# Kernel optimization log

Measured on AMD Instinct MI355X. Metric: run time of the kernel, lower is better.

The kernel has to match this reference:

```python
import jax, jax.numpy as jnp
import numpy as np

H, K, D, HID, B = 8, 2048, 64, 1024, 8192
TEMP = 1.0
LN_EPS = 1e-5


def setup_inputs() -> dict:
    key = jax.random.key(0)
    ks = jax.random.split(key, 6)
    s = lambda k, shape, scale=0.02: jax.random.normal(k, shape, jnp.float32) * scale
    return dict(
        z=jax.random.normal(ks[0], (B, HID), jnp.float32),
        w1=s(ks[1], (H, HID, 2 * D)),
        b1=jnp.zeros((H, 2 * D), jnp.float32),
        w2=s(ks[2], (H, 2 * D, D)),
        b2=jnp.zeros((H, D), jnp.float32),
        ln_g=jnp.ones((H, D), jnp.float32),
        ln_b=jnp.zeros((H, D), jnp.float32),
        codebooks=jax.random.normal(ks[3], (H, K, D), jnp.float32) * 0.1,
        dec_w=s(ks[4], (H, D, HID // H)),
        dec_b=jnp.zeros((H, HID // H), jnp.float32),
    )


def reference(z, w1, b1, w2, b2, ln_g, ln_b, codebooks, dec_w, dec_b):
    sg = jax.lax.stop_gradient
    Bf = z.shape[0]
    # per-head projection MLP (all heads fused via einsum): [B,HID] -> [B,H,2D] -> [B,H,D]
    h1 = jax.nn.gelu(jnp.einsum('bi,hio->bho', z, w1) + b1, approximate=False)
    zh = jnp.einsum('bho,hod->bhd', h1, w2) + b2
    mu = zh.mean(-1, keepdims=True)
    var = zh.var(-1, keepdims=True)  # biased, as torch LayerNorm
    z_heads = (zh - mu) / jnp.sqrt(var + LN_EPS) * ln_g + ln_b  # [B,H,D]
    # squared-distance to codebooks: ||z||^2 + ||c||^2 - 2 z.c  -> [B,H,K]
    z_sq = (z_heads ** 2).sum(-1)[..., None]          # [B,H,1]
    c_sq = (codebooks ** 2).sum(-1)[None]             # [1,H,K]
    zc = jnp.einsum('bhd,hkd->bhk', z_heads, codebooks)
    dists = z_sq + c_sq - 2.0 * zc
    idx = jnp.argmin(dists, axis=-1)                  # [B,H] int
    z_q = codebooks[jnp.arange(H)[None, :], idx]      # gather -> [B,H,D]
    # per-head decoders then concat -> [B,HID]
    dec = lambda x: (jnp.einsum('bhd,hdo->bho', x, dec_w) + dec_b).reshape(Bf, -1)
    z_q_dec = dec(z_q)
    z_proj = dec(z_heads)
    z_q_st = z_proj + sg(z_q_dec - z_proj)
    commit = jnp.mean((z_proj - sg(z_q_dec)) ** 2)
    codebook_loss = jnp.mean((sg(z_proj) - z_q_dec) ** 2)
    # entropy regularizer over soft assignment probs
    probs = jax.nn.softmax(-dists * TEMP, axis=-1)    # [B,H,K]
    avg_probs = probs.mean(0)                         # [H,K]
    entropy = -(avg_probs * jnp.log(avg_probs + 1e-8)).sum(-1).mean()
    entropy_loss = 1.0 - entropy / np.float32(np.log(K))
    # orthogonality: pairwise co-occurrence deviation from independence
    p = jnp.zeros((H, K), jnp.float32).at[jnp.arange(H)[None, :], idx].add(1.0) / Bf  # [H,K]
    ortho = jnp.float32(0.0)
    cnt = 0
    for i in range(H):
        for j in range(i + 1, H):
            co = jnp.zeros((K, K), jnp.float32).at[idx[:, i], idx[:, j]].add(1.0) / (Bf + 1e-8)
            expected = p[i][:, None] * p[j][None, :]
            ortho = ortho + jnp.mean(jnp.abs(co - expected))
            cnt += 1
    ortho = ortho / cnt
    return z_q_st, idx, commit, codebook_loss, entropy_loss, ortho, sg(z_heads)
```

## Files before the change

kernel.cpp:

```cpp
#include <hip/hip_runtime.h>
#include <math.h>

#define H 8
#define KK 2048
#define DD 64
#define HIDN 1024
#define BB 8192
#define TWO_D 128
#define OO 128

#define WS_CSQ   1048576
#define WS_ZSQ   1064960
#define WS_IDX   1130496
#define WS_AVGP  1196032
#define WS_HIST  1212416
#define WS_ACC   1228800
#define WS_ZERO_BYTES ((16384 + 16384 + 4) * 4)

#define OUT_ZQ 0
#define OUT_IDX 8388608
#define OUT_COMMIT 8454144
#define OUT_CBL 8454145
#define OUT_ENT 8454146
#define OUT_ORTHO 8454147
#define OUT_ZH 8454148
#define W2P_OFF 3145728

typedef __attribute__((ext_vector_type(8))) short bf16x8;
typedef __attribute__((ext_vector_type(4))) float f32x4;

__device__ inline unsigned short bf16_rne(float x) {
    union { float f; unsigned u; } c; c.f = x;
    unsigned r = c.u + 0x7FFFu + ((c.u >> 16) & 1u);
    return (unsigned short)(r >> 16);
}
__device__ inline float bf16_f32(unsigned short h) {
    union { unsigned u; float f; } c; c.u = ((unsigned)h) << 16;
    return c.f;
}
__device__ inline void split3(float x, short* hh, short* mm, short* ll) {
    unsigned short h_ = bf16_rne(x);
    float r1 = x - bf16_f32(h_);
    unsigned short m_ = bf16_rne(r1);
    float r2 = r1 - bf16_f32(m_);
    unsigned short l_ = bf16_rne(r2);
    *hh = (short)h_; *mm = (short)m_; *ll = (short)l_;
}

__device__ inline void gload_lds16(const void* g, void* l) {
    __builtin_amdgcn_global_load_lds(
        (const __attribute__((address_space(1))) unsigned int*)g,
        (__attribute__((address_space(3))) unsigned int*)l, 16, 0, 0);
}

__global__ __launch_bounds__(256) void k_pre_w1(const float* __restrict__ w1, float* outp) {
    short* w1p = (short*)outp;
    int h = blockIdx.x >> 5, kc = blockIdx.x & 31;
    int t = threadIdx.x;
    int l = t & 63, w = t >> 6;
    int lb = l & 15, lg = l >> 4;
#pragma unroll
    for (int oi = 0; oi < 2; ++oi) {
        int ot = w + oi * 4;
        union { short e[8]; bf16x8 v; } uh, um, ul;
#pragma unroll
        for (int j = 0; j < 8; ++j) {
            float x = w1[(size_t)(h * HIDN + kc * 32 + lg * 8 + j) * TWO_D + ot * 16 + lb];
            split3(x, &uh.e[j], &um.e[j], &ul.e[j]);
        }
        size_t base = (((size_t)(h * 32 + kc) * 8 + ot) * 3) * 512 + l * 8;
        *(bf16x8*)(w1p + base) = uh.v;
        *(bf16x8*)(w1p + base + 512) = um.v;
        *(bf16x8*)(w1p + base + 1024) = ul.v;
    }
}

__global__ __launch_bounds__(256) void k_pre_w2(const float* __restrict__ w2, float* outp) {
    short* w2p = (short*)outp + W2P_OFF;
    int h = blockIdx.x;
    int t = threadIdx.x;
    int l = t & 63, w = t >> 6;
    int lb = l & 15, lg = l >> 4;
#pragma unroll
    for (int i = 0; i < 4; ++i) {
        int fr = w * 4 + i;
        int dt = fr >> 2, oc = fr & 3;
        union { short e[8]; bf16x8 v; } uh, um, ul;
#pragma unroll
        for (int j = 0; j < 8; ++j) {
            float x = w2[(size_t)(h * TWO_D + oc * 32 + lg * 8 + j) * DD + dt * 16 + lb];
            split3(x, &uh.e[j], &um.e[j], &ul.e[j]);
        }
        size_t base = (((size_t)(h * 4 + dt) * 4 + oc) * 3) * 512 + l * 8;
        *(bf16x8*)(w2p + base) = uh.v;
        *(bf16x8*)(w2p + base + 512) = um.v;
        *(bf16x8*)(w2p + base + 1024) = ul.v;
    }
}

__global__ __launch_bounds__(256) void k_pre(const float* __restrict__ cb, float* __restrict__ ws) {
    int h = blockIdx.x >> 3, kb = blockIdx.x & 7;
    int t = threadIdx.x;
    int l = t & 63;
    int lb = l & 15, lg = l >> 4;
    short* stg = (short*)ws;
#pragma unroll
    for (int p = 0; p < 4; ++p) {
        int T = kb * 16 + p * 4 + (t >> 6);
        int k = T * 16 + lb;
        const float* row = cb + (size_t)(h * KK + k) * DD;
        float4 a0 = *(const float4*)(row + lg * 8);
        float4 a1 = *(const float4*)(row + lg * 8 + 4);
        float4 c0 = *(const float4*)(row + 32 + lg * 8);
        float4 c1 = *(const float4*)(row + 32 + lg * 8 + 4);
        float v0[8] = {a0.x, a0.y, a0.z, a0.w, a1.x, a1.y, a1.z, a1.w};
        float v1[8] = {c0.x, c0.y, c0.z, c0.w, c1.x, c1.y, c1.z, c1.w};
        union { short e[8]; bf16x8 v; } h0, h1;
        float s = 0.f;
#pragma unroll
        for (int j = 0; j < 8; ++j) {
            float x = v0[j];
            s = fmaf(x, x, s);
            h0.e[j] = (short)bf16_rne(x);
            float y = v1[j];
            s = fmaf(y, y, s);
            h1.e[j] = (short)bf16_rne(y);
        }
        size_t base = ((size_t)(h * 128 + T)) * 1024 + l * 8;
        *(bf16x8*)(stg + base) = h0.v;
        *(bf16x8*)(stg + base + 512) = h1.v;
        s += __shfl_xor(s, 16);
        s += __shfl_xor(s, 32);
        if (lg == 0) ws[WS_CSQ + h * KK + k] = s;
    }
}

__global__ __launch_bounds__(512, 4) void k1(const float* __restrict__ z, const float* __restrict__ b1,
                                             const float* __restrict__ b2, const float* __restrict__ lng,
                                             const float* __restrict__ lnb, float* out,
                                             float* __restrict__ ws) {
    __shared__ char SM[51200];
    int t = threadIdx.x;
    int h = blockIdx.y;
    int b0 = blockIdx.x * 64;
    int w = t >> 6, l = t & 63;
    int rg = w >> 1, wc = w & 1;
    int lb = l & 15, lg = l >> 4;

    const short* w2p = (const short*)out + W2P_OFF;
    const char* w1h = (const char*)out + (size_t)h * (32 * 24576);
    const float* zrow = z + (size_t)(b0 + rg * 16 + lb) * HIDN + lg * 8;

    {
        char* lb0 = SM + (t >> 6) * 1024;
        const char* gb = w1h + t * 16;
#pragma unroll
        for (int r = 0; r < 3; ++r) gload_lds16(gb + r * 8192, lb0 + r * 8192);
#pragma unroll
        for (int r = 0; r < 3; ++r) gload_lds16(gb + 24576 + r * 8192, lb0 + 24576 + r * 8192);
    }
    float4 zA = *(const float4*)(zrow);
    float4 zB = *(const float4*)(zrow + 4);
    __syncthreads();

    f32x4 acc[4];
#pragma unroll
    for (int i = 0; i < 4; ++i) acc[i] = (f32x4){0.f, 0.f, 0.f, 0.f};

#pragma unroll
    for (int c = 0; c < 32; ++c) {
        if (c > 0) {
            if (c < 31) asm volatile("s_waitcnt vmcnt(3)" ::: "memory");
            else        asm volatile("s_waitcnt vmcnt(0)" ::: "memory");
            __builtin_amdgcn_sched_barrier(0);
            __builtin_amdgcn_s_barrier();
            __builtin_amdgcn_sched_barrier(0);
        }
        {
            float zc[8] = {zA.x, zA.y, zA.z, zA.w, zB.x, zB.y, zB.z, zB.w};
            union { short e[8]; bf16x8 v; } uh, um, ul;
#pragma unroll
            for (int j = 0; j < 8; ++j) split3(zc[j], &uh.e[j], &um.e[j], &ul.e[j]);
            bf16x8 bh = uh.v, bm = um.v, blo = ul.v;
            const char* bp = SM + (c & 1) * 24576;
#pragma unroll
            for (int ot = 0; ot < 4; ++ot) {
                const char* fb = bp + (wc * 4 + ot) * 3072 + l * 16;
                bf16x8 ah = *(const bf16x8*)(fb);
                bf16x8 am = *(const bf16x8*)(fb + 1024);
                bf16x8 al = *(const bf16x8*)(fb + 2048);
                f32x4 cc = acc[ot];
                cc = __builtin_amdgcn_mfma_f32_16x16x32_bf16(ah, bh, cc, 0, 0, 0);
                cc = __builtin_amdgcn_mfma_f32_16x16x32_bf16(ah, bm, cc, 0, 0, 0);
                cc = __builtin_amdgcn_mfma_f32_16x16x32_bf16(am, bh, cc, 0, 0, 0);
                cc = __builtin_amdgcn_mfma_f32_16x16x32_bf16(ah, blo, cc, 0, 0, 0);
                cc = __builtin_amdgcn_mfma_f32_16x16x32_bf16(al, bh, cc, 0, 0, 0);
                cc = __builtin_amdgcn_mfma_f32_16x16x32_bf16(am, bm, cc, 0, 0, 0);
                acc[ot] = cc;
            }
        }
        __builtin_amdgcn_sched_barrier(0);
        __builtin_amdgcn_s_barrier();
        __builtin_amdgcn_sched_barrier(0);
        if (c < 31) {
            zA = *(const float4*)(zrow + (c + 1) * 32);
            zB = *(const float4*)(zrow + (c + 1) * 32 + 4);
        }
        if (c + 2 < 32) {
            char* lb0 = SM + (c & 1) * 24576 + (t >> 6) * 1024;
            const char* gb = w1h + (size_t)(c + 2) * 24576 + t * 16;
#pragma unroll
            for (int r = 0; r < 3; ++r) gload_lds16(gb + r * 8192, lb0 + r * 8192);
        }
    }
    __syncthreads();

    float* h1L = (float*)SM;
    float* zhL = (float*)(SM + 33792);

#pragma unroll
    for (int ot = 0; ot < 4; ++ot)
#pragma unroll
        for (int r = 0; r < 4; ++r) {
            int o = (wc * 4 + ot) * 16 + lg * 4 + r;
            float x = acc[ot][r] + b1[h * TWO_D + o];
            float gl = 0.5f * x * (1.0f + erff(x * 0.70710678118654752f));
            h1L[(rg * 16 + lb) * 132 + o] = gl;
        }
    __syncthreads();

    f32x4 a2[2];
    a2[0] = (f32x4){0.f, 0.f, 0.f, 0.f};
    a2[1] = (f32x4){0.f, 0.f, 0.f, 0.f};
#pragma unroll
    for (int oc = 0; oc < 4; ++oc) {
        const float* hr = h1L + (rg * 16 + lb) * 132 + oc * 32 + lg * 8;
        union { short e[8]; bf16x8 v; } uh, um, ul;
#pragma unroll
        for (int j = 0; j < 8; ++j) split3(hr[j], &uh.e[j], &um.e[j], &ul.e[j]);
        bf16x8 bh = uh.v, bm = um.v, blo = ul.v;
#pragma unroll
        for (int dti = 0; dti < 2; ++dti) {
            int dt = wc * 2 + dti;
            const short* fb = w2p + (((size_t)(h * 4 + dt) * 4 + oc) * 3) * 512 + l * 8;
            bf16x8 ah = *(const bf16x8*)(fb);
            bf16x8 am = *(const bf16x8*)(fb + 512);
            bf16x8 al = *(const bf16x8*)(fb + 1024);
            f32x4 cc = a2[dti];
            cc = __builtin_amdgcn_mfma_f32_16x16x32_bf16(ah, bh, cc, 0, 0, 0);
            cc = __builtin_amdgcn_mfma_f32_16x16x32_bf16(ah, bm, cc, 0, 0, 0);
            cc = __builtin_amdgcn_mfma_f32_16x16x32_bf16(am, bh, cc, 0, 0, 0);
            cc = __builtin_amdgcn_mfma_f32_16x16x32_bf16(ah, blo, cc, 0, 0, 0);
            cc = __builtin_amdgcn_mfma_f32_16x16x32_bf16(al, bh, cc, 0, 0, 0);
            cc = __builtin_amdgcn_mfma_f32_16x16x32_bf16(am, bm, cc, 0, 0, 0);
            a2[dti] = cc;
        }
    }
#pragma unroll
    for (int dti = 0; dti < 2; ++dti)
#pragma unroll
        for (int r = 0; r < 4; ++r) {
            int d = (wc * 2 + dti) * 16 + lg * 4 + r;
            zhL[(rg * 16 + lb) * 68 + d] = a2[dti][r] + b2[h * DD + d];
        }
    __syncthreads();

    {
        int row = t >> 3, c0 = (t & 7) * 8;
        const float* zr = zhL + row * 68 + c0;
        float v[8];
#pragma unroll
        for (int j = 0; j < 8; ++j) v[j] = zr[j];
        float s = 0.f;
#pragma unroll
        for (int j = 0; j < 8; ++j) s += v[j];
        s += __shfl_xor(s, 1); s += __shfl_xor(s, 2); s += __shfl_xor(s, 4);
        float mu = s * (1.0f / 64.0f);
        float vv = 0.f;
#pragma unroll
        for (int j = 0; j < 8; ++j) { float d = v[j] - mu; vv = fmaf(d, d, vv); }
        vv += __shfl_xor(vv, 1); vv += __shfl_xor(vv, 2); vv += __shfl_xor(vv, 4);
        float rstd = 1.0f / sqrtf(vv * (1.0f / 64.0f) + 1e-5f);
        float zn[8]; float ss = 0.f;
#pragma unroll
        for (int j = 0; j < 8; ++j) {
            float x = (v[j] - mu) * rstd * lng[h * DD + c0 + j] + lnb[h * DD + c0 + j];
            zn[j] = x; ss = fmaf(x, x, ss);
        }
        ss += __shfl_xor(ss, 1); ss += __shfl_xor(ss, 2); ss += __shfl_xor(ss, 4);
        int brow = b0 + row;
        if ((t & 7) == 0) ws[WS_ZSQ + brow * H + h] = ss;
        float4 s0 = {zn[0], zn[1], zn[2], zn[3]};
        float4 s1 = {zn[4], zn[5], zn[6], zn[7]};
        *(float4*)(out + OUT_ZH + (size_t)(brow * H + h) * DD + c0) = s0;
        *(float4*)(out + OUT_ZH + (size_t)(brow * H + h) * DD + c0 + 4) = s1;
    }
}

#define MARGIN 0.10f
__device__ inline void stage16(const char* gsrc, short* lbuf, int t) {
    char* lb_ = (char*)lbuf + (t >> 6) * 1024;
    gload_lds16(gsrc + t * 16, lb_);
}
__global__ __launch_bounds__(1024, 4) void k2(const float* __restrict__ cb,
                                              float* __restrict__ out, float* __restrict__ ws) {
    __shared__ short bufs[3][8192];
    __shared__ float zt[32][68];
    __shared__ float csqL[2048];
    __shared__ float zsqL[32];
    __shared__ float redM[8][32], redS[8][32], redE[8][32];
    __shared__ int   redK[8][32];
    __shared__ float MbL[32], SbL[32];
    __shared__ float paccL[2048];

    int t = threadIdx.x;
    int h = blockIdx.y;
    int b0 = blockIdx.x * 32;
    int w = t >> 6, l = t & 63;
    int rg = w >> 3, kg = w & 7;
    int lb = l & 15, lg = l >> 4;
    int rmy = rg * 16 + lb;

    const char* stgbase = (const char*)ws + (size_t)h * 262144;

    stage16(stgbase, bufs[0], t);
    stage16(stgbase + 16384, bufs[1], t);
    stage16(stgbase + 32768, bufs[2], t);
    for (int i = t; i < 2048; i += 1024) {
        paccL[i] = 0.f;
        csqL[i] = ws[WS_CSQ + h * KK + i];
    }
#pragma unroll
    for (int i = 0; i < 2; ++i) {
        int q = t + i * 1024;
        int r = q >> 6, d = q & 63;
        zt[r][d] = out[OUT_ZH + (size_t)((b0 + r) * H + h) * DD + d];
    }
    if (t < 32) zsqL[t] = ws[WS_ZSQ + (b0 + t) * H + h];
    __syncthreads();

    bf16x8 bh[2], bl[2];
#pragma unroll
    for (int s = 0; s < 2; ++s) {
        const float* zr = &zt[rmy][s * 32 + lg * 8];
        union { short e[8]; bf16x8 v; } uh, ul;
#pragma unroll
        for (int j = 0; j < 8; ++j) {
            float x = zr[j];
            unsigned short hb = bf16_rne(x);
            uh.e[j] = (short)hb;
            ul.e[j] = (short)bf16_rne(x - bf16_f32(hb));
        }
        bh[s] = uh.v; bl[s] = ul.v;
    }

    f32x4 acc[16];
#pragma unroll
    for (int a = 0; a < 16; ++a) acc[a] = (f32x4){0.f, 0.f, 0.f, 0.f};

#pragma unroll
    for (int c = 0; c < 16; ++c) {
        if (c > 0) {
            if (c <= 13)      asm volatile("s_waitcnt vmcnt(2)" ::: "memory");
            else if (c == 14) asm volatile("s_waitcnt vmcnt(1)" ::: "memory");
            else              asm volatile("s_waitcnt vmcnt(0)" ::: "memory");
            __builtin_amdgcn_sched_barrier(0);
            __builtin_amdgcn_s_barrier();
            __builtin_amdgcn_sched_barrier(0);
        }
        {
            const short* fb = bufs[c % 3] + kg * 1024 + l * 8;
            bf16x8 C0 = *(const bf16x8*)(fb);
            bf16x8 C1 = *(const bf16x8*)(fb + 512);
            f32x4 cc = acc[c];
            cc = __builtin_amdgcn_mfma_f32_16x16x32_bf16(bh[0], C0, cc, 0, 0, 0);
            cc = __builtin_amdgcn_mfma_f32_16x16x32_bf16(bl[0], C0, cc, 0, 0, 0);
            cc = __builtin_amdgcn_mfma_f32_16x16x32_bf16(bh[1], C1, cc, 0, 0, 0);
            cc = __builtin_amdgcn_mfma_f32_16x16x32_bf16(bl[1], C1, cc, 0, 0, 0);
            acc[c] = cc;
        }
        if (c < 15) {
            __builtin_amdgcn_sched_barrier(0);
            __builtin_amdgcn_s_barrier();
            __builtin_amdgcn_sched_barrier(0);
            if (c + 3 < 16)
                stage16(stgbase + (size_t)(c + 3) * 16384, bufs[c % 3], t);
        }
    }

    float zsqv[4];
#pragma unroll
    for (int r = 0; r < 4; ++r) zsqv[r] = zsqL[rg * 16 + lg * 4 + r];
    float mn[4] = {3.4e38f, 3.4e38f, 3.4e38f, 3.4e38f};
#pragma unroll
    for (int ai = 0; ai < 16; ++ai) {
        float cs = csqL[(8 * ai + kg) * 16 + lb];
        f32x4 a = acc[ai];
        f32x4 d;
#pragma unroll
        for (int r = 0; r < 4; ++r) {
            float dv = (zsqv[r] + cs) - 2.f * a[r];
            d[r] = dv;
            mn[r] = fminf(mn[r], dv);
        }
        acc[ai] = d;
    }
#pragma unroll
    for (int off = 1; off < 16; off <<= 1)
#pragma unroll
        for (int r = 0; r < 4; ++r) mn[r] = fminf(mn[r], __shfl_xor(mn[r], off));
    if (lb == 0)
#pragma unroll
        for (int r = 0; r < 4; ++r) redM[kg][rg * 16 + lg * 4 + r] = mn[r];
    __syncthreads();
    if (t < 32) {
        float m = redM[0][t];
#pragma unroll
        for (int g = 1; g < 8; ++g) m = fminf(m, redM[g][t]);
        MbL[t] = m;
    }
    __syncthreads();
    float Mb[4];
#pragma unroll
    for (int r = 0; r < 4; ++r) Mb[r] = MbL[rg * 16 + lg * 4 + r];

    float S[4] = {0.f, 0.f, 0.f, 0.f};
    unsigned mk0 = 0, mk1 = 0, mk2 = 0, mk3 = 0;
#pragma unroll
    for (int ai = 0; ai < 16; ++ai) {
        f32x4 d = acc[ai];
        f32x4 e;
#pragma unroll
        for (int r = 0; r < 4; ++r) {
            float dv = d[r];
            float ev = __expf(Mb[r] - dv);
            S[r] += ev;
            e[r] = ev;
            bool cand = dv <= Mb[r] + MARGIN;
            if (r == 0) mk0 |= cand ? (1u << ai) : 0u;
            if (r == 1) mk1 |= cand ? (1u << ai) : 0u;
            if (r == 2) mk2 |= cand ? (1u << ai) : 0u;
            if (r == 3) mk3 |= cand ? (1u << ai) : 0u;
        }
        acc[ai] = e;
    }
#pragma unroll
    for (int off = 1; off < 16; off <<= 1)
#pragma unroll
        for (int r = 0; r < 4; ++r) S[r] += __shfl_xor(S[r], off);
    if (lb == 0)
#pragma unroll
        for (int r = 0; r < 4; ++r) redS[kg][rg * 16 + lg * 4 + r] = S[r];

    float eB[4] = {3.4e38f, 3.4e38f, 3.4e38f, 3.4e38f};
    int kB[4] = {0x7FFFFFFF, 0x7FFFFFFF, 0x7FFFFFFF, 0x7FFFFFFF};
#pragma unroll
    for (int r = 0; r < 4; ++r) {
        unsigned m = (r == 0) ? mk0 : (r == 1) ? mk1 : (r == 2) ? mk2 : mk3;
        const float* zr0 = &zt[rg * 16 + lg * 4 + r][0];
        float eBest = 3.4e38f; int kBest = 0x7FFFFFFF;
        while (m) {
            int ai = (int)__ffs(m) - 1;
            m &= m - 1;
            int k = (8 * ai + kg) * 16 + lb;
            const float4* crow = (const float4*)(cb + (size_t)(h * KK + k) * DD);
            float s = 0.f;
#pragma unroll 1
            for (int q = 0; q < 16; ++q) {
                float4 cv = crow[q];
                s = fmaf(zr0[q * 4 + 0], cv.x, s);
                s = fmaf(zr0[q * 4 + 1], cv.y, s);
                s = fmaf(zr0[q * 4 + 2], cv.z, s);
                s = fmaf(zr0[q * 4 + 3], cv.w, s);
            }
            float ex = (zsqv[r] + csqL[k]) - 2.f * s;
            if (ex < eBest || (ex == eBest && k < kBest)) { eBest = ex; kBest = k; }
        }
        eB[r] = eBest; kB[r] = kBest;
    }
#pragma unroll
    for (int off = 1; off < 16; off <<= 1)
#pragma unroll
        for (int r = 0; r < 4; ++r) {
            float oe = __shfl_xor(eB[r], off);
            int ok = __shfl_xor(kB[r], off);
            if (oe < eB[r] || (oe == eB[r] && ok < kB[r])) { eB[r] = oe; kB[r] = ok; }
        }
    if (lb == 0)
#pragma unroll
        for (int r = 0; r < 4; ++r) {
            redE[kg][rg * 16 + lg * 4 + r] = eB[r];
            redK[kg][rg * 16 + lg * 4 + r] = kB[r];
        }
    __syncthreads();
    if (t < 32) {
        float Sv = redS[0][t];
#pragma unroll
        for (int g = 1; g < 8; ++g) Sv += redS[g][t];
        SbL[t] = Sv;
        float e0 = redE[0][t]; int k0_ = redK[0][t];
#pragma unroll
        for (int g = 1; g < 8; ++g) {
            float oe = redE[g][t]; int ok = redK[g][t];
            if (oe < e0 || (oe == e0 && ok < k0_)) { e0 = oe; k0_ = ok; }
        }
        out[OUT_IDX + (b0 + t) * H + h] = (float)k0_;
        ((int*)ws)[WS_IDX + (b0 + t) * H + h] = k0_;
        atomicAdd(((unsigned*)ws) + WS_HIST + h * KK + k0_, 1u);
    }
    __syncthreads();
    float invS[4];
#pragma unroll
    for (int r = 0; r < 4; ++r) invS[r] = 1.0f / SbL[rg * 16 + lg * 4 + r];

#pragma unroll
    for (int ai = 0; ai < 16; ++ai) {
        f32x4 e = acc[ai];
        float v = e[0] * invS[0];
        v = fmaf(e[1], invS[1], v);
        v = fmaf(e[2], invS[2], v);
        v = fmaf(e[3], invS[3], v);
        v += __shfl_xor(v, 16);
        v += __shfl_xor(v, 32);
        if (lg == 0) atomicAdd(&paccL[(8 * ai + kg) * 16 + lb], v);
    }
    __syncthreads();
    for (int i = t; i < 2048; i += 1024)
        atomicAdd(ws + WS_AVGP + h * KK + i, paccL[i]);
}

__global__ __launch_bounds__(256, 2) void k3(const float* __restrict__ cb, const float* __restrict__ dw,
                                             const float* __restrict__ db, float* __restrict__ out,
                                             float* __restrict__ ws) {
    __shared__ float zqt[32][65];
    __shared__ float zht[32][65];
    __shared__ float dwt[64][128];
    __shared__ int idxs[32];
    __shared__ double redc[4];
    int t = threadIdx.x;
    int h = blockIdx.y;
    int b0 = blockIdx.x * 32;
    if (t < 32) idxs[t] = ((const int*)ws)[WS_IDX + (b0 + t) * H + h];
    __syncthreads();
#pragma unroll
    for (int p = 0; p < 8; ++p) {
        int q = t + 256 * p;
        int r = q >> 6, d = q & 63;
        zqt[r][d] = cb[(size_t)(h * KK + idxs[r]) * DD + d];
        zht[r][d] = out[OUT_ZH + (size_t)((b0 + r) * H + h) * DD + d];
    }
#pragma unroll
    for (int p = 0; p < 8; ++p) {
        int q = t + 256 * p;
        int r = q >> 5, c4 = q & 31;
        *(float4*)(&dwt[r][c4 * 4]) = *(const float4*)(dw + (size_t)(h * DD + r) * OO + c4 * 4);
    }
    __syncthreads();
    int rg = t >> 4, cg = t & 15;
    float aq[2][8], ap[2][8];
#pragma unroll
    for (int i = 0; i < 2; ++i)
#pragma unroll
        for (int j = 0; j < 8; ++j) { aq[i][j] = 0.f; ap[i][j] = 0.f; }
#pragma unroll 4
    for (int d = 0; d < 64; ++d) {
        float q0 = zqt[rg * 2][d], q1 = zqt[rg * 2 + 1][d];
        float p0 = zht[rg * 2][d], p1 = zht[rg * 2 + 1][d];
        float4 wa = *(const float4*)(&dwt[d][cg * 8]);
        float4 wb = *(const float4*)(&dwt[d][cg * 8 + 4]);
        float ww[8] = {wa.x, wa.y, wa.z, wa.w, wb.x, wb.y, wb.z, wb.w};
#pragma unroll
        for (int j = 0; j < 8; ++j) {
            aq[0][j] = fmaf(q0, ww[j], aq[0][j]);
            aq[1][j] = fmaf(q1, ww[j], aq[1][j]);
            ap[0][j] = fmaf(p0, ww[j], ap[0][j]);
            ap[1][j] = fmaf(p1, ww[j], ap[1][j]);
        }
    }
    float lsum = 0.f;
#pragma unroll
    for (int i = 0; i < 2; ++i) {
        float vq4[8];
#pragma unroll
        for (int j = 0; j < 8; ++j) {
            float bb = db[h * OO + cg * 8 + j];
            float vq = aq[i][j] + bb;
            float vp = ap[i][j] + bb;
            vq4[j] = vp + (vq - vp);
            float e = vp - vq;
            lsum = fmaf(e, e, lsum);
        }
        float4 s0 = {vq4[0], vq4[1], vq4[2], vq4[3]};
        float4 s1 = {vq4[4], vq4[5], vq4[6], vq4[7]};
        size_t o = (size_t)(b0 + rg * 2 + i) * HIDN + h * OO + cg * 8;
        *(float4*)(out + OUT_ZQ + o) = s0;
        *(float4*)(out + OUT_ZQ + o + 4) = s1;
    }
#pragma unroll
    for (int off = 1; off < 64; off <<= 1) lsum += __shfl_xor(lsum, off);
    if ((t & 63) == 0) redc[t >> 6] = (double)lsum;
    __syncthreads();
    if (t == 0) atomicAdd((double*)(ws + WS_ACC), redc[0] + redc[1] + redc[2] + redc[3]);
}

__global__ __launch_bounds__(256) void k6(float* __restrict__ ws) {
    __shared__ unsigned slots[16384];
    __shared__ unsigned cnts[16384];
    int t = threadIdx.x;
    int bid = blockIdx.x;
    int pi = 0, pj = 1;
    {
        int c = 0;
        for (int a = 0; a < H; ++a)
            for (int b = a + 1; b < H; ++b) { if (c == bid) { pi = a; pj = b; } ++c; }
    }
    for (int s = t; s < 16384; s += 256) { slots[s] = 0xFFFFFFFFu; cnts[s] = 0u; }
    __syncthreads();
    const int* idxi = ((const int*)ws) + WS_IDX;
    for (int b = t; b < BB; b += 256) {
        unsigned key = ((unsigned)idxi[b * H + pi] << 11) | (unsigned)idxi[b * H + pj];
        unsigned p = (key * 2654435761u) >> 18;
        while (true) {
            unsigned old = atomicCAS(&slots[p], 0xFFFFFFFFu, key);
            if (old == 0xFFFFFFFFu || old == key) { atomicAdd(&cnts[p], 1u); break; }
            p = (p + 1) & 16383u;
        }
    }
    __syncthreads();
    const unsigned* hist = ((const unsigned*)ws) + WS_HIST;
    double loc = 0.0;
    for (int s = t; s < 16384; s += 256) {
        unsigned key = slots[s];
        if (key != 0xFFFFFFFFu) {
            int ki = (int)(key >> 11), kj = (int)(key & 2047u);
            float c = (float)cnts[s] * (1.0f / 8192.0f);
            float piv = (float)hist[pi * KK + ki] * (1.0f / 8192.0f);
            float pjv = (float)hist[pj * KK + kj] * (1.0f / 8192.0f);
            float e = piv * pjv;
            loc += (double)fabsf(c - e) - (double)e;
        }
    }
    double spi = 0.0, spj = 0.0;
    for (int k = t; k < KK; k += 256) {
        spi += (double)hist[pi * KK + k];
        spj += (double)hist[pj * KK + k];
    }
#pragma unroll
    for (int off = 1; off < 64; off <<= 1) {
        loc += __shfl_xor(loc, off);
        spi += __shfl_xor(spi, off);
        spj += __shfl_xor(spj, off);
    }
    __syncthreads();
    double* sc = (double*)cnts;
    if ((t & 63) == 0) { int w = t >> 6; sc[w] = loc; sc[4 + w] = spi; sc[8 + w] = spj; }
    __syncthreads();
    if (t == 0) {
        double L = sc[0] + sc[1] + sc[2] + sc[3];
        double SPI = (sc[4] + sc[5] + sc[6] + sc[7]) / 8192.0;
        double SPJ = (sc[8] + sc[9] + sc[10] + sc[11]) / 8192.0;
        atomicAdd(((double*)(ws + WS_ACC)) + 1, L + SPI * SPJ);
    }
}

__global__ __launch_bounds__(256) void k4(float* __restrict__ out, float* __restrict__ ws) {
    __shared__ double red[256];
    int t = threadIdx.x;
    double tot = 0.0;
    for (int h = 0; h < H; ++h) {
        double s = 0.0;
        for (int k = t; k < KK; k += 256) {
            double a = (double)ws[WS_AVGP + h * KK + k] / 8192.0;
            s += a * log(a + 1e-8);
        }
        tot += s;
    }
    red[t] = tot;
    __syncthreads();
    for (int off = 128; off; off >>= 1) {
        if (t < off) red[t] += red[t + off];
        __syncthreads();
    }
    if (t == 0) {
        double entropy = -red[0] / 8.0;
        out[OUT_ENT] = (float)(1.0 - entropy / log(2048.0));
        double ca = *(const double*)(ws + WS_ACC);
        float cm = (float)(ca / (8192.0 * 1024.0));
        out[OUT_COMMIT] = cm;
        out[OUT_CBL] = cm;
        double oa = *(((const double*)(ws + WS_ACC)) + 1);
        out[OUT_ORTHO] = (float)(oa / (28.0 * 4194304.0));
    }
}

extern "C" void kernel_launch(void* const* d_in, const int* in_sizes, int n_in,
                              void* d_out, int out_size, void* d_ws, size_t ws_size,
                              hipStream_t stream) {
    (void)in_sizes; (void)n_in; (void)out_size; (void)ws_size;
    const float* z   = (const float*)d_in[0];
    const float* w1  = (const float*)d_in[1];
    const float* b1  = (const float*)d_in[2];
    const float* w2  = (const float*)d_in[3];
    const float* b2  = (const float*)d_in[4];
    const float* lng = (const float*)d_in[5];
    const float* lnb = (const float*)d_in[6];
    const float* cb  = (const float*)d_in[7];
    const float* dw  = (const float*)d_in[8];
    const float* db  = (const float*)d_in[9];
    float* out = (float*)d_out;
    float* ws = (float*)d_ws;

    hipMemsetAsync(ws + WS_AVGP, 0, WS_ZERO_BYTES, stream);
    k_pre_w1<<<256, 256, 0, stream>>>(w1, out);
    k_pre_w2<<<8, 256, 0, stream>>>(w2, out);
    k_pre<<<64, 256, 0, stream>>>(cb, ws);
    k1<<<dim3(128, 8), 512, 0, stream>>>(z, b1, b2, lng, lnb, out, ws);
    k2<<<dim3(256, 8), 1024, 0, stream>>>(cb, out, ws);
    k3<<<dim3(256, 8), 256, 0, stream>>>(cb, dw, db, out, ws);
    k6<<<28, 256, 0, stream>>>(ws);
    k4<<<1, 256, 0, stream>>>(out, ws);
}
```

Before: 537.4 us.

## Shrink k2 blocks to 16 rows, drop LDS staging, move histogram to separate kernel

The distance/argmin kernel now uses 512-thread blocks covering 16 batch rows, with twice as many blocks. Each thread issues two async loads per stage, and the staged codebook layout is permuted so each wave owns a contiguous 256-code range. Codebook norms are read from global memory instead of an LDS copy, the LDS soft-probability accumulator is replaced by direct global atomics, and the MFMA block runs at raised priority. The per-row global histogram atomics move into a new per-head kernel with an LDS histogram. This lowers LDS use and raises occupancy, but the codebook is re-streamed once per block for half as many rows, so staged codebook traffic doubles, global atomics increase, and one more launch is added.

```diff
diff --git a/kernel.cpp b/kernel.cpp
--- a/kernel.cpp
+++ b/kernel.cpp
@@ -126,7 +126,8 @@
             s = fmaf(y, y, s);
             h1.e[j] = (short)bf16_rne(y);
         }
-        size_t base = ((size_t)(h * 128 + T)) * 1024 + l * 8;
+        int off = (T & 15) * 8 + (T >> 4);
+        size_t base = ((size_t)(h * 128 + off)) * 1024 + l * 8;
         *(bf16x8*)(stg + base) = h0.v;
         *(bf16x8*)(stg + base + 512) = h1.v;
         s += __shfl_xor(s, 16);
@@ -298,51 +299,45 @@
 }
 
 #define MARGIN 0.10f
-__device__ inline void stage16(const char* gsrc, short* lbuf, int t) {
+__device__ inline void stage16k(const char* gsrc, short* lbuf, int t) {
     char* lb_ = (char*)lbuf + (t >> 6) * 1024;
-    gload_lds16(gsrc + t * 16, lb_);
-}
-__global__ __launch_bounds__(1024, 4) void k2(const float* __restrict__ cb,
-                                              float* __restrict__ out, float* __restrict__ ws) {
+    const char* gb = gsrc + t * 16;
+    gload_lds16(gb, lb_);
+    gload_lds16(gb + 8192, lb_ + 8192);
+}
+__global__ __launch_bounds__(512, 4) void k2(const float* __restrict__ cb,
+                                             float* __restrict__ out, float* __restrict__ ws) {
     __shared__ short bufs[3][8192];
-    __shared__ float zt[32][68];
-    __shared__ float csqL[2048];
-    __shared__ float zsqL[32];
-    __shared__ float redM[8][32], redS[8][32], redE[8][32];
-    __shared__ int   redK[8][32];
-    __shared__ float MbL[32], SbL[32];
-    __shared__ float paccL[2048];
+    __shared__ float zt[16][68];
+    __shared__ float redM[8][16], redS[8][16], redE[8][16];
+    __shared__ int   redK[8][16];
+    __shared__ float MbL[16], SbL[16];
+    __shared__ float zsqL[16];
 
     int t = threadIdx.x;
     int h = blockIdx.y;
-    int b0 = blockIdx.x * 32;
-    int w = t >> 6, l = t & 63;
-    int rg = w >> 3, kg = w & 7;
+    int b0 = blockIdx.x * 16;
+    int kg = t >> 6, l = t & 63;
     int lb = l & 15, lg = l >> 4;
-    int rmy = rg * 16 + lb;
 
     const char* stgbase = (const char*)ws + (size_t)h * 262144;
 
-    stage16(stgbase, bufs[0], t);
-    stage16(stgbase + 16384, bufs[1], t);
-    stage16(stgbase + 32768, bufs[2], t);
-    for (int i = t; i < 2048; i += 1024) {
-        paccL[i] = 0.f;
-        csqL[i] = ws[WS_CSQ + h * KK + i];
-    }
+    stage16k(stgbase, bufs[0], t);
+    stage16k(stgbase + 16384, bufs[1], t);
+    stage16k(stgbase + 32768, bufs[2], t);
 #pragma unroll
     for (int i = 0; i < 2; ++i) {
-        int q = t + i * 1024;
+        int q = t + i * 512;
         int r = q >> 6, d = q & 63;
         zt[r][d] = out[OUT_ZH + (size_t)((b0 + r) * H + h) * DD + d];
     }
-    if (t < 32) zsqL[t] = ws[WS_ZSQ + (b0 + t) * H + h];
-    __syncthreads();
-
-    bf16x8 bh[2], bl[2];
+    if (t < 16) zsqL[t] = ws[WS_ZSQ + (b0 + t) * H + h];
+    __syncthreads();
+
+    bf16x8 bh[2], blo[2];
 #pragma unroll
     for (int s = 0; s < 2; ++s) {
-        const float* zr = &zt[rmy][s * 32 + lg * 8];
+        const float* zr = &zt[lb][s * 32 + lg * 8];
         union { short e[8]; bf16x8 v; } uh, ul;
 #pragma unroll
         for (int j = 0; j < 8; ++j) {
@@ -351,7 +346,7 @@
             uh.e[j] = (short)hb;
             ul.e[j] = (short)bf16_rne(x - bf16_f32(hb));
         }
-        bh[s] = uh.v; bl[s] = ul.v;
+        bh[s] = uh.v; blo[s] = ul.v;
     }
 
     f32x4 acc[16];
@@ -361,8 +356,8 @@
 #pragma unroll
     for (int c = 0; c < 16; ++c) {
         if (c > 0) {
-            if (c <= 13)      asm volatile("s_waitcnt vmcnt(2)" ::: "memory");
-            else if (c == 14) asm volatile("s_waitcnt vmcnt(1)" ::: "memory");
+            if (c <= 13)      asm volatile("s_waitcnt vmcnt(4)" ::: "memory");
+            else if (c == 14) asm volatile("s_waitcnt vmcnt(2)" ::: "memory");
             else              asm volatile("s_waitcnt vmcnt(0)" ::: "memory");
             __builtin_amdgcn_sched_barrier(0);
             __builtin_amdgcn_s_barrier();
@@ -373,10 +368,12 @@
             bf16x8 C0 = *(const bf16x8*)(fb);
             bf16x8 C1 = *(const bf16x8*)(fb + 512);
             f32x4 cc = acc[c];
+            __builtin_amdgcn_s_setprio(1);
             cc = __builtin_amdgcn_mfma_f32_16x16x32_bf16(bh[0], C0, cc, 0, 0, 0);
-            cc = __builtin_amdgcn_mfma_f32_16x16x32_bf16(bl[0], C0, cc, 0, 0, 0);
+            cc = __builtin_amdgcn_mfma_f32_16x16x32_bf16(blo[0], C0, cc, 0, 0, 0);
             cc = __builtin_amdgcn_mfma_f32_16x16x32_bf16(bh[1], C1, cc, 0, 0, 0);
-            cc = __builtin_amdgcn_mfma_f32_16x16x32_bf16(bl[1], C1, cc, 0, 0, 0);
+            cc = __builtin_amdgcn_mfma_f32_16x16x32_bf16(blo[1], C1, cc, 0, 0, 0);
+            __builtin_amdgcn_s_setprio(0);
             acc[c] = cc;
         }
         if (c < 15) {
@@ -384,17 +381,17 @@
             __builtin_amdgcn_s_barrier();
             __builtin_amdgcn_sched_barrier(0);
             if (c + 3 < 16)
-                stage16(stgbase + (size_t)(c + 3) * 16384, bufs[c % 3], t);
+                stage16k(stgbase + (size_t)(c + 3) * 16384, bufs[c % 3], t);
         }
     }
 
     float zsqv[4];
 #pragma unroll
-    for (int r = 0; r < 4; ++r) zsqv[r] = zsqL[rg * 16 + lg * 4 + r];
+    for (int r = 0; r < 4; ++r) zsqv[r] = zsqL[lg * 4 + r];
     float mn[4] = {3.4e38f, 3.4e38f, 3.4e38f, 3.4e38f};
 #pragma unroll
     for (int ai = 0; ai < 16; ++ai) {
-        float cs = csqL[(8 * ai + kg) * 16 + lb];
+        float cs = ws[WS_CSQ + h * KK + kg * 256 + ai * 16 + lb];
         f32x4 a = acc[ai];
         f32x4 d;
 #pragma unroll
@@ -411,9 +408,9 @@
         for (int r = 0; r < 4; ++r) mn[r] = fminf(mn[r], __shfl_xor(mn[r], off));
     if (lb == 0)
 #pragma unroll
-        for (int r = 0; r < 4; ++r) redM[kg][rg * 16 + lg * 4 + r] = mn[r];
-    __syncthreads();
-    if (t < 32) {
+        for (int r = 0; r < 4; ++r) redM[kg][lg * 4 + r] = mn[r];
+    __syncthreads();
+    if (t < 16) {
         float m = redM[0][t];
 #pragma unroll
         for (int g = 1; g < 8; ++g) m = fminf(m, redM[g][t]);
@@ -422,7 +419,7 @@
     __syncthreads();
     float Mb[4];
 #pragma unroll
-    for (int r = 0; r < 4; ++r) Mb[r] = MbL[rg * 16 + lg * 4 + r];
+    for (int r = 0; r < 4; ++r) Mb[r] = MbL[lg * 4 + r];
 
     float S[4] = {0.f, 0.f, 0.f, 0.f};
     unsigned mk0 = 0, mk1 = 0, mk2 = 0, mk3 = 0;
@@ -450,19 +447,19 @@
         for (int r = 0; r < 4; ++r) S[r] += __shfl_xor(S[r], off);
     if (lb == 0)
 #pragma unroll
-        for (int r = 0; r < 4; ++r) redS[kg][rg * 16 + lg * 4 + r] = S[r];
+        for (int r = 0; r < 4; ++r) redS[kg][lg * 4 + r] = S[r];
 
     float eB[4] = {3.4e38f, 3.4e38f, 3.4e38f, 3.4e38f};
     int kB[4] = {0x7FFFFFFF, 0x7FFFFFFF, 0x7FFFFFFF, 0x7FFFFFFF};
 #pragma unroll
     for (int r = 0; r < 4; ++r) {
         unsigned m = (r == 0) ? mk0 : (r == 1) ? mk1 : (r == 2) ? mk2 : mk3;
-        const float* zr0 = &zt[rg * 16 + lg * 4 + r][0];
+        const float* zr0 = &zt[lg * 4 + r][0];
         float eBest = 3.4e38f; int kBest = 0x7FFFFFFF;
         while (m) {
             int ai = (int)__ffs(m) - 1;
             m &= m - 1;
-            int k = (8 * ai + kg) * 16 + lb;
+            int k = kg * 256 + ai * 16 + lb;
             const float4* crow = (const float4*)(cb + (size_t)(h * KK + k) * DD);
             float s = 0.f;
 #pragma unroll 1
@@ -473,7 +470,7 @@
                 s = fmaf(zr0[q * 4 + 2], cv.z, s);
                 s = fmaf(zr0[q * 4 + 3], cv.w, s);
             }
-            float ex = (zsqv[r] + csqL[k]) - 2.f * s;
+            float ex = (zsqv[r] + ws[WS_CSQ + h * KK + k]) - 2.f * s;
             if (ex < eBest || (ex == eBest && k < kBest)) { eBest = ex; kBest = k; }
         }
         eB[r] = eBest; kB[r] = kBest;
@@ -489,11 +486,11 @@
     if (lb == 0)
 #pragma unroll
         for (int r = 0; r < 4; ++r) {
-            redE[kg][rg * 16 + lg * 4 + r] = eB[r];
-            redK[kg][rg * 16 + lg * 4 + r] = kB[r];
-        }
-    __syncthreads();
-    if (t < 32) {
+            redE[kg][lg * 4 + r] = eB[r];
+            redK[kg][lg * 4 + r] = kB[r];
+        }
+    __syncthreads();
+    if (t < 16) {
         float Sv = redS[0][t];
 #pragma unroll
         for (int g = 1; g < 8; ++g) Sv += redS[g][t];
@@ -506,12 +503,11 @@
         }
         out[OUT_IDX + (b0 + t) * H + h] = (float)k0_;
         ((int*)ws)[WS_IDX + (b0 + t) * H + h] = k0_;
-        atomicAdd(((unsigned*)ws) + WS_HIST + h * KK + k0_, 1u);
     }
     __syncthreads();
     float invS[4];
 #pragma unroll
-    for (int r = 0; r < 4; ++r) invS[r] = 1.0f / SbL[rg * 16 + lg * 4 + r];
+    for (int r = 0; r < 4; ++r) invS[r] = 1.0f / SbL[lg * 4 + r];
 
 #pragma unroll
     for (int ai = 0; ai < 16; ++ai) {
@@ -522,11 +518,22 @@
         v = fmaf(e[3], invS[3], v);
         v += __shfl_xor(v, 16);
         v += __shfl_xor(v, 32);
-        if (lg == 0) atomicAdd(&paccL[(8 * ai + kg) * 16 + lb], v);
-    }
-    __syncthreads();
-    for (int i = t; i < 2048; i += 1024)
-        atomicAdd(ws + WS_AVGP + h * KK + i, paccL[i]);
+        if (lg == 0)
+            atomicAdd(ws + WS_AVGP + h * KK + kg * 256 + ai * 16 + lb, v);
+    }
+}
+
+__global__ __launch_bounds__(256) void k_hist(float* __restrict__ ws) {
+    __shared__ unsigned hl[2048];
+    int h = blockIdx.x, t = threadIdx.x;
+    for (int i = t; i < 2048; i += 256) hl[i] = 0u;
+    __syncthreads();
+    const int* idxi = ((const int*)ws) + WS_IDX;
+    for (int b = t; b < BB; b += 256)
+        atomicAdd(&hl[idxi[b * H + h]], 1u);
+    __syncthreads();
+    for (int i = t; i < 2048; i += 256)
+        ((unsigned*)ws)[WS_HIST + h * KK + i] = hl[i];
 }
 
 __global__ __launch_bounds__(256, 2) void k3(const float* __restrict__ cb, const float* __restrict__ dw,
@@ -715,7 +722,8 @@
     k_pre_w2<<<8, 256, 0, stream>>>(w2, out);
     k_pre<<<64, 256, 0, stream>>>(cb, ws);
     k1<<<dim3(128, 8), 512, 0, stream>>>(z, b1, b2, lng, lnb, out, ws);
-    k2<<<dim3(256, 8), 1024, 0, stream>>>(cb, out, ws);
+    k2<<<dim3(512, 8), 512, 0, stream>>>(cb, out, ws);
+    k_hist<<<8, 256, 0, stream>>>(ws);
     k3<<<dim3(256, 8), 256, 0, stream>>>(cb, dw, db, out, ws);
     k6<<<28, 256, 0, stream>>>(ws);
     k4<<<1, 256, 0, stream>>>(out, ws);
```

After: 568.3 us. 5.7% more time.

## Load split-bf16 codebook fragments directly to registers and move histogram to separate kernel

Applied to the files above, without the earlier changes.

The codebook distance kernel stops staging codebook tiles through LDS with barriers. Each wave now reads pre-split hi/lo bf16 fragments straight from global memory into registers with a two-deep prefetch, and adds a third MFMA term (z_hi·c_lo) to raise precision, which allows a tighter refinement margin. The soft-probability accumulation moves ahead of the exact argmin refinement, and the global histogram atomics are replaced by a small per-head shared-memory histogram kernel. In exchange the staging buffer doubles, MFMA work per tile grows by half, and csq is read from global memory instead of LDS.

```diff
diff --git a/kernel.cpp b/kernel.cpp
--- a/kernel.cpp
+++ b/kernel.cpp
@@ -115,20 +115,26 @@
         float4 c1 = *(const float4*)(row + 32 + lg * 8 + 4);
         float v0[8] = {a0.x, a0.y, a0.z, a0.w, a1.x, a1.y, a1.z, a1.w};
         float v1[8] = {c0.x, c0.y, c0.z, c0.w, c1.x, c1.y, c1.z, c1.w};
-        union { short e[8]; bf16x8 v; } h0, h1;
+        union { short e[8]; bf16x8 v; } h0, h1, l0, l1;
         float s = 0.f;
 #pragma unroll
         for (int j = 0; j < 8; ++j) {
             float x = v0[j];
             s = fmaf(x, x, s);
-            h0.e[j] = (short)bf16_rne(x);
+            unsigned short hb = bf16_rne(x);
+            h0.e[j] = (short)hb;
+            l0.e[j] = (short)bf16_rne(x - bf16_f32(hb));
             float y = v1[j];
             s = fmaf(y, y, s);
-            h1.e[j] = (short)bf16_rne(y);
-        }
-        size_t base = ((size_t)(h * 128 + T)) * 1024 + l * 8;
+            unsigned short hb2 = bf16_rne(y);
+            h1.e[j] = (short)hb2;
+            l1.e[j] = (short)bf16_rne(y - bf16_f32(hb2));
+        }
+        size_t base = ((size_t)(h * 128 + T)) * 2048 + l * 8;
         *(bf16x8*)(stg + base) = h0.v;
         *(bf16x8*)(stg + base + 512) = h1.v;
+        *(bf16x8*)(stg + base + 1024) = l0.v;
+        *(bf16x8*)(stg + base + 1536) = l1.v;
         s += __shfl_xor(s, 16);
         s += __shfl_xor(s, 32);
         if (lg == 0) ws[WS_CSQ + h * KK + k] = s;
@@ -297,21 +303,15 @@
     }
 }
 
-#define MARGIN 0.10f
-__device__ inline void stage16(const char* gsrc, short* lbuf, int t) {
-    char* lb_ = (char*)lbuf + (t >> 6) * 1024;
-    gload_lds16(gsrc + t * 16, lb_);
-}
+#define MARGIN 0.05f
 __global__ __launch_bounds__(1024, 4) void k2(const float* __restrict__ cb,
                                               float* __restrict__ out, float* __restrict__ ws) {
-    __shared__ short bufs[3][8192];
     __shared__ float zt[32][68];
-    __shared__ float csqL[2048];
-    __shared__ float zsqL[32];
+    __shared__ float paccL[2048];
     __shared__ float redM[8][32], redS[8][32], redE[8][32];
     __shared__ int   redK[8][32];
     __shared__ float MbL[32], SbL[32];
-    __shared__ float paccL[2048];
+    __shared__ float zsqL[32];
 
     int t = threadIdx.x;
     int h = blockIdx.y;
@@ -321,15 +321,7 @@
     int lb = l & 15, lg = l >> 4;
     int rmy = rg * 16 + lb;
 
-    const char* stgbase = (const char*)ws + (size_t)h * 262144;
-
-    stage16(stgbase, bufs[0], t);
-    stage16(stgbase + 16384, bufs[1], t);
-    stage16(stgbase + 32768, bufs[2], t);
-    for (int i = t; i < 2048; i += 1024) {
-        paccL[i] = 0.f;
-        csqL[i] = ws[WS_CSQ + h * KK + i];
-    }
+    for (int i = t; i < 2048; i += 1024) paccL[i] = 0.f;
 #pragma unroll
     for (int i = 0; i < 2; ++i) {
         int q = t + i * 1024;
@@ -339,7 +331,7 @@
     if (t < 32) zsqL[t] = ws[WS_ZSQ + (b0 + t) * H + h];
     __syncthreads();
 
-    bf16x8 bh[2], bl[2];
+    bf16x8 bh[2], blo[2];
 #pragma unroll
     for (int s = 0; s < 2; ++s) {
         const float* zr = &zt[rmy][s * 32 + lg * 8];
@@ -351,40 +343,41 @@
             uh.e[j] = (short)hb;
             ul.e[j] = (short)bf16_rne(x - bf16_f32(hb));
         }
-        bh[s] = uh.v; bl[s] = ul.v;
-    }
+        bh[s] = uh.v; blo[s] = ul.v;
+    }
+
+    const short* tbase = (const short*)ws + ((size_t)(h * 128 + kg * 16)) * 2048 + l * 8;
 
     f32x4 acc[16];
 #pragma unroll
     for (int a = 0; a < 16; ++a) acc[a] = (f32x4){0.f, 0.f, 0.f, 0.f};
 
-#pragma unroll
-    for (int c = 0; c < 16; ++c) {
-        if (c > 0) {
-            if (c <= 13)      asm volatile("s_waitcnt vmcnt(2)" ::: "memory");
-            else if (c == 14) asm volatile("s_waitcnt vmcnt(1)" ::: "memory");
-            else              asm volatile("s_waitcnt vmcnt(0)" ::: "memory");
-            __builtin_amdgcn_sched_barrier(0);
-            __builtin_amdgcn_s_barrier();
-            __builtin_amdgcn_sched_barrier(0);
-        }
-        {
-            const short* fb = bufs[c % 3] + kg * 1024 + l * 8;
-            bf16x8 C0 = *(const bf16x8*)(fb);
-            bf16x8 C1 = *(const bf16x8*)(fb + 512);
-            f32x4 cc = acc[c];
-            cc = __builtin_amdgcn_mfma_f32_16x16x32_bf16(bh[0], C0, cc, 0, 0, 0);
-            cc = __builtin_amdgcn_mfma_f32_16x16x32_bf16(bl[0], C0, cc, 0, 0, 0);
-            cc = __builtin_amdgcn_mfma_f32_16x16x32_bf16(bh[1], C1, cc, 0, 0, 0);
-            cc = __builtin_amdgcn_mfma_f32_16x16x32_bf16(bl[1], C1, cc, 0, 0, 0);
-            acc[c] = cc;
-        }
-        if (c < 15) {
-            __builtin_amdgcn_sched_barrier(0);
-            __builtin_amdgcn_s_barrier();
-            __builtin_amdgcn_sched_barrier(0);
-            if (c + 3 < 16)
-                stage16(stgbase + (size_t)(c + 3) * 16384, bufs[c % 3], t);
+    bf16x8 c0h, c1h, c0l, c1l, p0h, p1h, p0l, p1l;
+    c0h = *(const bf16x8*)(tbase);
+    c1h = *(const bf16x8*)(tbase + 512);
+    c0l = *(const bf16x8*)(tbase + 1024);
+    c1l = *(const bf16x8*)(tbase + 1536);
+    p0h = *(const bf16x8*)(tbase + 2048);
+    p1h = *(const bf16x8*)(tbase + 2048 + 512);
+    p0l = *(const bf16x8*)(tbase + 2048 + 1024);
+    p1l = *(const bf16x8*)(tbase + 2048 + 1536);
+#pragma unroll
+    for (int ai = 0; ai < 16; ++ai) {
+        f32x4 cc = acc[ai];
+        cc = __builtin_amdgcn_mfma_f32_16x16x32_bf16(bh[0], c0h, cc, 0, 0, 0);
+        cc = __builtin_amdgcn_mfma_f32_16x16x32_bf16(blo[0], c0h, cc, 0, 0, 0);
+        cc = __builtin_amdgcn_mfma_f32_16x16x32_bf16(bh[0], c0l, cc, 0, 0, 0);
+        cc = __builtin_amdgcn_mfma_f32_16x16x32_bf16(bh[1], c1h, cc, 0, 0, 0);
+        cc = __builtin_amdgcn_mfma_f32_16x16x32_bf16(blo[1], c1h, cc, 0, 0, 0);
+        cc = __builtin_amdgcn_mfma_f32_16x16x32_bf16(bh[1], c1l, cc, 0, 0, 0);
+        acc[ai] = cc;
+        c0h = p0h; c1h = p1h; c0l = p0l; c1l = p1l;
+        if (ai + 2 < 16) {
+            const short* np = tbase + (size_t)(ai + 2) * 2048;
+            p0h = *(const bf16x8*)(np);
+            p1h = *(const bf16x8*)(np + 512);
+            p0l = *(const bf16x8*)(np + 1024);
+            p1l = *(const bf16x8*)(np + 1536);
         }
     }
 
@@ -394,7 +387,7 @@
     float mn[4] = {3.4e38f, 3.4e38f, 3.4e38f, 3.4e38f};
 #pragma unroll
     for (int ai = 0; ai < 16; ++ai) {
-        float cs = csqL[(8 * ai + kg) * 16 + lb];
+        float cs = ws[WS_CSQ + h * KK + (kg * 16 + ai) * 16 + lb];
         f32x4 a = acc[ai];
         f32x4 d;
 #pragma unroll
@@ -451,6 +444,30 @@
     if (lb == 0)
 #pragma unroll
         for (int r = 0; r < 4; ++r) redS[kg][rg * 16 + lg * 4 + r] = S[r];
+    __syncthreads();
+    if (t < 32) {
+        float Sv = redS[0][t];
+#pragma unroll
+        for (int g = 1; g < 8; ++g) Sv += redS[g][t];
+        SbL[t] = Sv;
+    }
+    __syncthreads();
+    float invS[4];
+#pragma unroll
+    for (int r = 0; r < 4; ++r) invS[r] = 1.0f / SbL[rg * 16 + lg * 4 + r];
+
+#pragma unroll
+    for (int ai = 0; ai < 16; ++ai) {
+        f32x4 e = acc[ai];
+        float v = e[0] * invS[0];
+        v = fmaf(e[1], invS[1], v);
+        v = fmaf(e[2], invS[2], v);
+        v = fmaf(e[3], invS[3], v);
+        v += __shfl_xor(v, 16);
+        v += __shfl_xor(v, 32);
+        if (lg == 0)
+            atomicAdd(&paccL[(kg * 16 + ai) * 16 + lb], v);
+    }
 
     float eB[4] = {3.4e38f, 3.4e38f, 3.4e38f, 3.4e38f};
     int kB[4] = {0x7FFFFFFF, 0x7FFFFFFF, 0x7FFFFFFF, 0x7FFFFFFF};
@@ -462,7 +479,7 @@
         while (m) {
             int ai = (int)__ffs(m) - 1;
             m &= m - 1;
-            int k = (8 * ai + kg) * 16 + lb;
+            int k = (kg * 16 + ai) * 16 + lb;
             const float4* crow = (const float4*)(cb + (size_t)(h * KK + k) * DD);
             float s = 0.f;
 #pragma unroll 1
@@ -473,7 +490,7 @@
                 s = fmaf(zr0[q * 4 + 2], cv.z, s);
                 s = fmaf(zr0[q * 4 + 3], cv.w, s);
             }
-            float ex = (zsqv[r] + csqL[k]) - 2.f * s;
+            float ex = (zsqv[r] + ws[WS_CSQ + h * KK + k]) - 2.f * s;
             if (ex < eBest || (ex == eBest && k < kBest)) { eBest = ex; kBest = k; }
         }
         eB[r] = eBest; kB[r] = kBest;
@@ -494,10 +511,6 @@
         }
     __syncthreads();
     if (t < 32) {
-        float Sv = redS[0][t];
-#pragma unroll
-        for (int g = 1; g < 8; ++g) Sv += redS[g][t];
-        SbL[t] = Sv;
         float e0 = redE[0][t]; int k0_ = redK[0][t];
 #pragma unroll
         for (int g = 1; g < 8; ++g) {
@@ -506,27 +519,23 @@
         }
         out[OUT_IDX + (b0 + t) * H + h] = (float)k0_;
         ((int*)ws)[WS_IDX + (b0 + t) * H + h] = k0_;
-        atomicAdd(((unsigned*)ws) + WS_HIST + h * KK + k0_, 1u);
-    }
-    __syncthreads();
-    float invS[4];
-#pragma unroll
-    for (int r = 0; r < 4; ++r) invS[r] = 1.0f / SbL[rg * 16 + lg * 4 + r];
-
-#pragma unroll
-    for (int ai = 0; ai < 16; ++ai) {
-        f32x4 e = acc[ai];
-        float v = e[0] * invS[0];
-        v = fmaf(e[1], invS[1], v);
-        v = fmaf(e[2], invS[2], v);
-        v = fmaf(e[3], invS[3], v);
-        v += __shfl_xor(v, 16);
-        v += __shfl_xor(v, 32);
-        if (lg == 0) atomicAdd(&paccL[(8 * ai + kg) * 16 + lb], v);
     }
     __syncthreads();
     for (int i = t; i < 2048; i += 1024)
         atomicAdd(ws + WS_AVGP + h * KK + i, paccL[i]);
+}
+
+__global__ __launch_bounds__(256) void k_hist(float* __restrict__ ws) {
+    __shared__ unsigned hl[2048];
+    int h = blockIdx.x, t = threadIdx.x;
+    for (int i = t; i < 2048; i += 256) hl[i] = 0u;
+    __syncthreads();
+    const int* idxi = ((const int*)ws) + WS_IDX;
+    for (int b = t; b < BB; b += 256)
+        atomicAdd(&hl[idxi[b * H + h]], 1u);
+    __syncthreads();
+    for (int i = t; i < 2048; i += 256)
+        ((unsigned*)ws)[WS_HIST + h * KK + i] = hl[i];
 }
 
 __global__ __launch_bounds__(256, 2) void k3(const float* __restrict__ cb, const float* __restrict__ dw,
@@ -716,6 +725,7 @@
     k_pre<<<64, 256, 0, stream>>>(cb, ws);
     k1<<<dim3(128, 8), 512, 0, stream>>>(z, b1, b2, lng, lnb, out, ws);
     k2<<<dim3(256, 8), 1024, 0, stream>>>(cb, out, ws);
+    k_hist<<<8, 256, 0, stream>>>(ws);
     k3<<<dim3(256, 8), 256, 0, stream>>>(cb, dw, db, out, ws);
     k6<<<28, 256, 0, stream>>>(ws);
     k4<<<1, 256, 0, stream>>>(out, ws);
```

New measurement: 659.8 us. 22.8% more time.
